# Kernel tuning notes

Measured on AMD Instinct MI355X. Metric: run time of the kernel, lower is better.

The kernel has to match this reference:

```python
import jax, jax.numpy as jnp
import numpy as np

N = 100000   # nodes of ntype 'gene'
E = 800000   # edges per metapath
D = 256      # input_dim == output_dim
H = 4        # attn heads
C = D // H   # out_channels per head
M = 2        # num metapaths (tail relations = M + 1, last = self)


def _lrelu(x):
    return jnp.where(x >= 0, x, 0.2 * x)


def _segment_softmax(logits, seg, num_segments):
    # logits: [E, H], seg: [E] int targets
    mx = jax.ops.segment_max(logits, seg, num_segments=num_segments)
    mx = jnp.where(jnp.isfinite(mx), mx, 0.0)  # empty segments -> 0
    ex = jnp.exp(logits - mx[seg])
    den = jax.ops.segment_sum(ex, seg, num_segments=num_segments)
    return ex / (den[seg] + 1e-16)


def setup_inputs() -> dict:
    key = jax.random.key(0)
    ks = jax.random.split(key, 10)
    s = 1.0 / np.sqrt(D)
    return {
        "x": jax.random.normal(ks[0], (N, D), dtype=jnp.float32),
        "edge_index0": jax.random.randint(ks[1], (2, E), 0, N, dtype=jnp.int32),
        "edge_index1": jax.random.randint(ks[2], (2, E), 0, N, dtype=jnp.int32),
        "W_l": jax.random.normal(ks[3], (D, D), dtype=jnp.float32) * s,
        "b_l": jnp.zeros((D,), dtype=jnp.float32),
        "W_r": jax.random.normal(ks[4], (D, D), dtype=jnp.float32) * s,
        "b_r": jnp.zeros((D,), dtype=jnp.float32),
        "attn": jax.random.normal(ks[5], (M, H, 2 * C), dtype=jnp.float32) * (1.0 / np.sqrt(2 * C)),
        "rel_attn_l": jax.random.normal(ks[6], (H, C), dtype=jnp.float32) * (1.0 / np.sqrt(C)),
        "rel_attn_r": jax.random.normal(ks[7], (H, C), dtype=jnp.float32) * (1.0 / np.sqrt(C)),
    }


def reference(x, edge_index0, edge_index1, W_l, b_l, W_r, b_r, attn, rel_attn_l, rel_attn_r):
    # projections -> [N, H, C]  (eval mode: dropout/batchnorm off)
    l = (x @ W_l.T + b_l).reshape(N, H, C)
    r = (x @ W_r.T + b_r).reshape(N, H, C)

    # attn split: first C for x_i (target, r-proj), last C for x_j (source, l-proj);
    # leaky_relu is elementwise so the concat+dot separates exactly.
    def agg(edge_index, m_idx):
        src, tgt = edge_index[0], edge_index[1]
        a_i = jnp.einsum('ehc,hc->eh', _lrelu(r[tgt]), attn[m_idx, :, :C])
        a_j = jnp.einsum('ehc,hc->eh', _lrelu(l[src]), attn[m_idx, :, C:])
        alpha = _segment_softmax(a_i + a_j, tgt, N)          # [E, H]
        msg = l[src] * alpha[:, :, None]                      # [E, H, C]
        return jax.ops.segment_sum(msg, tgt, num_segments=N)  # [N, H, C]

    out0 = agg(edge_index0, 0)
    out1 = agg(edge_index1, 1)
    emb = jnp.stack([out0, out1, r], axis=1)                  # [N, M+1, H, C]

    # relation-level beta attention (get_beta_weights)
    alpha_l = jnp.einsum('nhc,hc->nh', r, rel_attn_l)         # [N, H]
    alpha_r = jnp.einsum('nrhc,hc->nrh', emb, rel_attn_r)     # [N, M+1, H]
    beta = jax.nn.softmax(_lrelu(alpha_l[:, None, :] + alpha_r), axis=1)

    h = (emb * beta[..., None]).sum(axis=1).reshape(N, D)
    return jax.nn.relu(h)
```

## Files before the change

kernel.cpp:

```cpp
#include <hip/hip_runtime.h>
#include <hip/hip_bf16.h>
#include <math.h>

#define D_ 256
#define H_ 4
#define C_ 64

typedef __attribute__((ext_vector_type(8))) short short8;
typedef __attribute__((ext_vector_type(4))) float f32x4;

__device__ inline float lrelu(float v) { return v >= 0.f ? v : 0.2f * v; }

__device__ inline unsigned short f2b(float f) {
    unsigned u = __float_as_uint(f);
    u = (u + 0x7FFFu + ((u >> 16) & 1u)) >> 16;
    return (unsigned short)u;
}
__device__ inline float b2f(unsigned short u) {
    return __uint_as_float(((unsigned)u) << 16);
}

#define GLDS(src, dst) __builtin_amdgcn_global_load_lds(                      \
    (const __attribute__((address_space(1))) void*)(src),                     \
    (__attribute__((address_space(3))) void*)(dst), 16, 0, 0)

__global__ __launch_bounds__(256) void convert_w(
    const float* __restrict__ Wl, const float* __restrict__ Wr,
    unsigned short* __restrict__ Wb)
{
    int i4 = blockIdx.x * 256 + threadIdx.x;
    float4 v = (i4 < 16384) ? ((const float4*)Wl)[i4]
                            : ((const float4*)Wr)[i4 - 16384];
    ushort4 u;
    u.x = f2b(v.x); u.y = f2b(v.y); u.z = f2b(v.z); u.w = f2b(v.w);
    ((ushort4*)Wb)[i4] = u;
}

__device__ __forceinline__ void stage_a(const float* __restrict__ x, float* dst,
                                        int bm, int k0, int wv, int lane, int Mrows)
{
#pragma unroll
    for (int p = 0; p < 4; p++) {
        int ci = (p * 4 + wv) * 64 + lane;
        int row = ci >> 3, cc = ci & 7;
        int gr = bm + row; if (gr >= Mrows) gr = Mrows - 1;
        const float* src = x + (size_t)gr * 256 + k0 + ((cc ^ (row & 7)) << 2);
        GLDS(src, (char*)dst + (size_t)(p * 4 + wv) * 1024);
    }
}
__device__ __forceinline__ void stage_b(const unsigned short* __restrict__ W,
                                        unsigned short* dst, int bn, int k0,
                                        int wv, int lane)
{
#pragma unroll
    for (int p = 0; p < 2; p++) {
        int ci = (p * 4 + wv) * 64 + lane;
        int col = ci >> 2, cc = ci & 3;
        const unsigned short* src = W + (size_t)(bn + col) * 256 + k0 +
                                    ((cc ^ (col & 3)) << 3);
        GLDS(src, (char*)dst + (size_t)(p * 4 + wv) * 1024);
    }
}

__global__ __launch_bounds__(256) void gemm_fused(
    const float* __restrict__ x, const unsigned short* __restrict__ Wb,
    const float* __restrict__ b_l, const float* __restrict__ b_r,
    unsigned short* __restrict__ lout, float* __restrict__ rout, int Mrows)
{
    __shared__ float As[2][128 * 32];
    __shared__ unsigned short Bs[2][128 * 32];
    const int tid = threadIdx.x;
    const int lane = tid & 63, wv = tid >> 6;
    const int wr = wv >> 1, wc = wv & 1;
    const int sel = blockIdx.x >> 1;
    const int bn = (blockIdx.x & 1) * 128;
    const int bm = blockIdx.y * 128;
    const unsigned short* W = Wb + (size_t)sel * 65536;

    f32x4 acc[4][4];
#pragma unroll
    for (int m = 0; m < 4; m++)
#pragma unroll
        for (int n = 0; n < 4; n++) acc[m][n] = (f32x4)0.f;

    stage_a(x, As[0], bm, 0, wv, lane, Mrows);
    stage_b(W, Bs[0], bn, 0, wv, lane);
    __syncthreads();

    int cur = 0;
#pragma unroll
    for (int t = 0; t < 8; t++) {
        if (t < 7) {
            stage_a(x, As[cur ^ 1], bm, (t + 1) * 32, wv, lane, Mrows);
            stage_b(W, Bs[cur ^ 1], bn, (t + 1) * 32, wv, lane);
        }
        short8 bfr[4];
#pragma unroll
        for (int n = 0; n < 4; n++) {
            int col = wc * 64 + n * 16 + (lane & 15);
            int sc = (lane >> 4) ^ (col & 3);
            bfr[n] = *(const short8*)&Bs[cur][col * 32 + sc * 8];
        }
        short8 afr[4];
#pragma unroll
        for (int m = 0; m < 4; m++) {
            int row = wr * 64 + m * 16 + (lane & 15);
            int c0 = (lane >> 4) * 2;
            const float* ap = &As[cur][row * 32];
            float4 f0 = *(const float4*)&ap[(c0 ^ (row & 7)) << 2];
            float4 f1 = *(const float4*)&ap[((c0 + 1) ^ (row & 7)) << 2];
            union { short8 v; __hip_bfloat162 b2[4]; } u;
            u.b2[0] = __float22bfloat162_rn(make_float2(f0.x, f0.y));
            u.b2[1] = __float22bfloat162_rn(make_float2(f0.z, f0.w));
            u.b2[2] = __float22bfloat162_rn(make_float2(f1.x, f1.y));
            u.b2[3] = __float22bfloat162_rn(make_float2(f1.z, f1.w));
            afr[m] = u.v;
        }
#pragma unroll
        for (int m = 0; m < 4; m++)
#pragma unroll
            for (int n = 0; n < 4; n++)
                acc[m][n] = __builtin_amdgcn_mfma_f32_16x16x32_bf16(
                    afr[m], bfr[n], acc[m][n], 0, 0, 0);
        __syncthreads();
        cur ^= 1;
    }

    const float* bias = sel ? b_r : b_l;
#pragma unroll
    for (int m = 0; m < 4; m++) {
        int grow0 = bm + wr * 64 + m * 16 + (lane >> 4) * 4;
#pragma unroll
        for (int n = 0; n < 4; n++) {
            int gcol = bn + wc * 64 + n * 16 + (lane & 15);
            float bv = bias[gcol];
#pragma unroll
            for (int q = 0; q < 4; q++) {
                int grow = grow0 + q;
                if (grow < Mrows) {
                    float v = acc[m][n][q] + bv;
                    if (sel == 0) lout[(size_t)grow * 256 + gcol] = f2b(v);
                    else          rout[(size_t)grow * 256 + gcol] = v;
                }
            }
        }
    }
}

__global__ __launch_bounds__(256) void node_logits(
    const unsigned short* __restrict__ l, const float* __restrict__ r,
    const float* __restrict__ attn, const float* __restrict__ rel_l,
    const float* __restrict__ rel_r,
    float2* __restrict__ ej2, float* __restrict__ al, float* __restrict__ rd,
    int Nn)
{
    int lane = threadIdx.x & 63;
    int n = blockIdx.x * 4 + (threadIdx.x >> 6);
    if (n >= Nn) return;
    int h = lane >> 4, q = lane & 15;

    ushort4 lv4 = *(const ushort4*)&l[(size_t)n * D_ + lane * 4];
    float4 rv4 = *(const float4*)&r[(size_t)n * D_ + lane * 4];
    float4 a0 = *(const float4*)&attn[(0 * H_ + h) * 128 + 64 + q * 4];
    float4 a1 = *(const float4*)&attn[(1 * H_ + h) * 128 + 64 + q * 4];
    float4 wl = *(const float4*)&rel_l[h * C_ + q * 4];
    float4 wr = *(const float4*)&rel_r[h * C_ + q * 4];

    float lf[4] = { b2f(lv4.x), b2f(lv4.y), b2f(lv4.z), b2f(lv4.w) };
    float rf[4] = { rv4.x, rv4.y, rv4.z, rv4.w };
    float af0[4] = { a0.x, a0.y, a0.z, a0.w };
    float af1[4] = { a1.x, a1.y, a1.z, a1.w };
    float wlf[4] = { wl.x, wl.y, wl.z, wl.w };
    float wrf[4] = { wr.x, wr.y, wr.z, wr.w };

    float v2 = 0.f, v3 = 0.f, v4 = 0.f, v5 = 0.f, v6 = 0.f;
#pragma unroll
    for (int k = 0; k < 4; k++) {
        float ll = lrelu(lf[k]);
        v2 = fmaf(ll, af0[k], v2);
        v3 = fmaf(ll, af1[k], v3);
        v4 = fmaf(rf[k], wlf[k], v4);
        v5 = fmaf(lf[k], wrf[k], v5);
        v6 = fmaf(rf[k], wrf[k], v6);
    }
#pragma unroll
    for (int off = 1; off < 16; off <<= 1) {
        v2 += __shfl_xor(v2, off);
        v3 += __shfl_xor(v3, off);
        v4 += __shfl_xor(v4, off);
        v5 += __shfl_xor(v5, off);
        v6 += __shfl_xor(v6, off);
    }
    if (q == 0) {
        int NH = Nn * H_;
        int nh = n * H_ + h;
        float e0 = __expf(v2), e1 = __expf(v3);
        ej2[nh]      = make_float2(e0, e0 * v5);
        ej2[NH + nh] = make_float2(e1, e1 * v5);
        al[nh] = v4;
        rd[nh] = v6;
    }
}

__global__ __launch_bounds__(256) void edge_hist(
    const int* __restrict__ ei0, const int* __restrict__ ei1,
    int* __restrict__ hist, int E_, int Nn)
{
    int e = blockIdx.x * 256 + threadIdx.x;
    if (e >= E_) return;
    atomicAdd(&hist[ei0[E_ + e]], 1);
    atomicAdd(&hist[Nn + ei1[E_ + e]], 1);
}

__global__ __launch_bounds__(256) void scan_a(
    const int* __restrict__ hist, int* __restrict__ segoff,
    int* __restrict__ bsum, int Nn)
{
    int m = blockIdx.y;
    int gid = blockIdx.x * 256 + threadIdx.x;
    int lane = threadIdx.x & 63, wid = threadIdx.x >> 6;
    int v = (gid < Nn) ? hist[m * Nn + gid] : 0;
    int incl = v;
#pragma unroll
    for (int off = 1; off < 64; off <<= 1) {
        int u = __shfl_up(incl, off);
        if (lane >= off) incl += u;
    }
    __shared__ int ws[4], wo[4];
    if (lane == 63) ws[wid] = incl;
    __syncthreads();
    if (threadIdx.x == 0) {
        int run = 0;
#pragma unroll
        for (int i = 0; i < 4; i++) { wo[i] = run; run += ws[i]; }
        bsum[m * 512 + blockIdx.x] = run;
    }
    __syncthreads();
    if (gid < Nn) segoff[m * Nn + gid] = incl - v + wo[wid];
}

__global__ __launch_bounds__(512) void scan_b(int* __restrict__ bsum, int nb)
{
    int m = blockIdx.x;
    int* b = bsum + m * 512;
    int tid = threadIdx.x, lane = tid & 63, wid = tid >> 6;
    int v = (tid < nb) ? b[tid] : 0;
    int incl = v;
#pragma unroll
    for (int off = 1; off < 64; off <<= 1) {
        int u = __shfl_up(incl, off);
        if (lane >= off) incl += u;
    }
    __shared__ int ws[8], wo[8];
    if (lane == 63) ws[wid] = incl;
    __syncthreads();
    if (tid == 0) {
        int run = 0;
#pragma unroll
        for (int i = 0; i < 8; i++) { wo[i] = run; run += ws[i]; }
    }
    __syncthreads();
    if (tid < nb) b[tid] = incl - v + wo[wid];
}

__global__ __launch_bounds__(256) void scan_c(
    int* __restrict__ segoff, const int* __restrict__ bsum, int Nn)
{
    int m = blockIdx.y;
    int gid = blockIdx.x * 256 + threadIdx.x;
    if (gid < Nn) segoff[m * Nn + gid] += bsum[m * 512 + blockIdx.x];
}

__global__ __launch_bounds__(256) void edge_scatter(
    const int* __restrict__ ei0, const int* __restrict__ ei1,
    const int* __restrict__ segoff, int* __restrict__ cursor,
    int* __restrict__ srcs, int E_, int Nn)
{
    int e = blockIdx.x * 256 + threadIdx.x;
    if (e >= E_) return;
    int t0 = ei0[E_ + e];
    int p0 = segoff[t0] + atomicAdd(&cursor[t0], 1);
    srcs[p0] = ei0[e];
    int t1 = ei1[E_ + e];
    int p1 = segoff[Nn + t1] + atomicAdd(&cursor[Nn + t1], 1);
    srcs[E_ + p1] = ei1[e];
}

__global__ __launch_bounds__(256) void aggregate(
    const int* __restrict__ hist, const int* __restrict__ segoff,
    const int* __restrict__ srcs, const float2* __restrict__ ej2,
    const float* __restrict__ al, const float* __restrict__ rd,
    const float* __restrict__ r, const unsigned short* __restrict__ l,
    float* __restrict__ out, int Nn, int E_)
{
    int lane = threadIdx.x & 63;
    int t = blockIdx.x * 4 + (threadIdx.x >> 6);
    if (t >= Nn) return;
    int h = lane >> 4, q = lane & 15;
    int NH = Nn * H_;
    int nh = t * H_ + h;

    int beg0 = segoff[t],      deg0 = hist[t];
    int beg1 = segoff[Nn + t], deg1 = hist[Nn + t];
    float den0 = 0.f, pn0 = 0.f, den1 = 0.f, pn1 = 0.f;
    for (int j = q; j < deg0; j += 16) {
        float2 v = ej2[(size_t)srcs[beg0 + j] * H_ + h];
        den0 += v.x; pn0 += v.y;
    }
    for (int j = q; j < deg1; j += 16) {
        float2 v = ej2[(size_t)NH + (size_t)srcs[E_ + beg1 + j] * H_ + h];
        den1 += v.x; pn1 += v.y;
    }
#pragma unroll
    for (int off = 1; off < 16; off <<= 1) {
        den0 += __shfl_xor(den0, off); pn0 += __shfl_xor(pn0, off);
        den1 += __shfl_xor(den1, off); pn1 += __shfl_xor(pn1, off);
    }

    float a = al[nh];
    float b0 = lrelu(a + pn0 / (den0 + 1e-16f));
    float b1 = lrelu(a + pn1 / (den1 + 1e-16f));
    float b2 = lrelu(a + rd[nh]);
    float mm = fmaxf(b0, fmaxf(b1, b2));
    float e0 = __expf(b0 - mm), e1 = __expf(b1 - mm), e2 = __expf(b2 - mm);
    float inv = 1.f / (e0 + e1 + e2);
    float wm0 = e0 * inv / (den0 + 1e-16f);
    float wm1 = e1 * inv / (den1 + 1e-16f);
    float b2v = e2 * inv;

    float4 acc = *(const float4*)&r[(size_t)t * D_ + lane * 4];
    acc.x *= b2v; acc.y *= b2v; acc.z *= b2v; acc.w *= b2v;

#pragma unroll
    for (int m = 0; m < 2; m++) {
        const int* sp = srcs + (size_t)m * E_;
        int beg = m ? beg1 : beg0;
        int deg = m ? deg1 : deg0;
        float wmv = m ? wm1 : wm0;
        const float2* ep = ej2 + (size_t)m * NH;
#pragma unroll 4
        for (int j = 0; j < deg; j++) {
            int s = sp[beg + j];
            float w = ep[(size_t)s * H_ + h].x * wmv;
            ushort4 lv = *(const ushort4*)&l[(size_t)s * D_ + lane * 4];
            acc.x = fmaf(b2f(lv.x), w, acc.x);
            acc.y = fmaf(b2f(lv.y), w, acc.y);
            acc.z = fmaf(b2f(lv.z), w, acc.z);
            acc.w = fmaf(b2f(lv.w), w, acc.w);
        }
    }
    float4 o;
    o.x = fmaxf(acc.x, 0.f); o.y = fmaxf(acc.y, 0.f);
    o.z = fmaxf(acc.z, 0.f); o.w = fmaxf(acc.w, 0.f);
    *(float4*)&out[(size_t)t * D_ + lane * 4] = o;
}

extern "C" void kernel_launch(void* const* d_in, const int* in_sizes, int n_in,
                              void* d_out, int out_size, void* d_ws, size_t ws_size,
                              hipStream_t stream) {
    const float* x     = (const float*)d_in[0];
    const int*   ei0   = (const int*)d_in[1];
    const int*   ei1   = (const int*)d_in[2];
    const float* W_l   = (const float*)d_in[3];
    const float* b_l   = (const float*)d_in[4];
    const float* W_r   = (const float*)d_in[5];
    const float* b_r   = (const float*)d_in[6];
    const float* attn  = (const float*)d_in[7];
    const float* rel_l = (const float*)d_in[8];
    const float* rel_r = (const float*)d_in[9];
    float* out = (float*)d_out;

    const int Nn = in_sizes[0] / D_;
    const int E_ = in_sizes[1] / 2;
    const size_t ND = (size_t)Nn * D_;
    const int NH = Nn * H_;

    char* base = (char*)d_ws;
    unsigned short* l = (unsigned short*)base;      size_t off = ND * 2;
    float2* ej2  = (float2*)(base + off); off += (size_t)2 * NH * 8;
    float* al    = (float*)(base + off);  off += (size_t)NH * 4;
    float* rd    = (float*)(base + off);  off += (size_t)NH * 4;
    int* hist    = (int*)(base + off);    off += (size_t)2 * Nn * 4;
    int* cursor  = (int*)(base + off);    off += (size_t)2 * Nn * 4;
    int* segoff  = (int*)(base + off);    off += (size_t)2 * Nn * 4;
    int* bsum    = (int*)(base + off);    off += (size_t)1024 * 4;
    int* srcs    = (int*)(base + off);    off += (size_t)2 * E_ * 4;
    unsigned short* Wb = (unsigned short*)(base + off); off += (size_t)2 * 65536 * 2;

    hipMemsetAsync(hist, 0, (size_t)4 * Nn * 4, stream);

    convert_w<<<128, 256, 0, stream>>>(W_l, W_r, Wb);

    int rowTiles = (Nn + 127) / 128;
    gemm_fused<<<dim3(4, rowTiles), 256, 0, stream>>>(x, Wb, b_l, b_r, l, out, Nn);

    node_logits<<<(Nn + 3) / 4, 256, 0, stream>>>(l, out, attn, rel_l, rel_r,
                                                  ej2, al, rd, Nn);

    int eb = (E_ + 255) / 256;
    int nb = (Nn + 255) / 256;
    edge_hist<<<eb, 256, 0, stream>>>(ei0, ei1, hist, E_, Nn);
    scan_a<<<dim3(nb, 2), 256, 0, stream>>>(hist, segoff, bsum, Nn);
    scan_b<<<2, 512, 0, stream>>>(bsum, nb);
    scan_c<<<dim3(nb, 2), 256, 0, stream>>>(segoff, bsum, Nn);
    edge_scatter<<<eb, 256, 0, stream>>>(ei0, ei1, segoff, cursor, srcs, E_, Nn);

    aggregate<<<(Nn + 3) / 4, 256, 0, stream>>>(
        hist, segoff, srcs, ej2, al, rd, out, l, out, Nn, E_);
}
```

Measured before the change: 482.5 us.

## Fuse softmax denominator pass into aggregation and store r projection as bf16

```diff
diff --git a/kernel.cpp b/kernel.cpp
--- a/kernel.cpp
+++ b/kernel.cpp
@@ -62,10 +62,11 @@
     }
 }
 
+template <bool RB16>
 __global__ __launch_bounds__(256) void gemm_fused(
     const float* __restrict__ x, const unsigned short* __restrict__ Wb,
     const float* __restrict__ b_l, const float* __restrict__ b_r,
-    unsigned short* __restrict__ lout, float* __restrict__ rout, int Mrows)
+    unsigned short* __restrict__ lout, void* __restrict__ rout, int Mrows)
 {
     __shared__ float As[2][128 * 32];
     __shared__ unsigned short Bs[2][128 * 32];
@@ -139,16 +140,21 @@
                 int grow = grow0 + q;
                 if (grow < Mrows) {
                     float v = acc[m][n][q] + bv;
-                    if (sel == 0) lout[(size_t)grow * 256 + gcol] = f2b(v);
-                    else          rout[(size_t)grow * 256 + gcol] = v;
+                    if (sel == 0) {
+                        lout[(size_t)grow * 256 + gcol] = f2b(v);
+                    } else {
+                        if (RB16) ((unsigned short*)rout)[(size_t)grow * 256 + gcol] = f2b(v);
+                        else      ((float*)rout)[(size_t)grow * 256 + gcol] = v;
+                    }
                 }
             }
         }
     }
 }
 
+template <bool RB16>
 __global__ __launch_bounds__(256) void node_logits(
-    const unsigned short* __restrict__ l, const float* __restrict__ r,
+    const unsigned short* __restrict__ l, const void* __restrict__ rv,
     const float* __restrict__ attn, const float* __restrict__ rel_l,
     const float* __restrict__ rel_r,
     float2* __restrict__ ej2, float* __restrict__ al, float* __restrict__ rd,
@@ -160,14 +166,20 @@
     int h = lane >> 4, q = lane & 15;
 
     ushort4 lv4 = *(const ushort4*)&l[(size_t)n * D_ + lane * 4];
-    float4 rv4 = *(const float4*)&r[(size_t)n * D_ + lane * 4];
+    float rf[4];
+    if (RB16) {
+        ushort4 ru = ((const ushort4*)rv)[(size_t)n * 64 + lane];
+        rf[0] = b2f(ru.x); rf[1] = b2f(ru.y); rf[2] = b2f(ru.z); rf[3] = b2f(ru.w);
+    } else {
+        float4 rv4 = ((const float4*)rv)[(size_t)n * 64 + lane];
+        rf[0] = rv4.x; rf[1] = rv4.y; rf[2] = rv4.z; rf[3] = rv4.w;
+    }
     float4 a0 = *(const float4*)&attn[(0 * H_ + h) * 128 + 64 + q * 4];
     float4 a1 = *(const float4*)&attn[(1 * H_ + h) * 128 + 64 + q * 4];
     float4 wl = *(const float4*)&rel_l[h * C_ + q * 4];
     float4 wr = *(const float4*)&rel_r[h * C_ + q * 4];
 
     float lf[4] = { b2f(lv4.x), b2f(lv4.y), b2f(lv4.z), b2f(lv4.w) };
-    float rf[4] = { rv4.x, rv4.y, rv4.z, rv4.w };
     float af0[4] = { a0.x, a0.y, a0.z, a0.w };
     float af1[4] = { a1.x, a1.y, a1.z, a1.w };
     float wlf[4] = { wl.x, wl.y, wl.z, wl.w };
@@ -286,35 +298,50 @@
     srcs[E_ + p1] = ei1[e];
 }
 
+template <bool RB16>
 __global__ __launch_bounds__(256) void aggregate(
     const int* __restrict__ hist, const int* __restrict__ segoff,
     const int* __restrict__ srcs, const float2* __restrict__ ej2,
     const float* __restrict__ al, const float* __restrict__ rd,
-    const float* __restrict__ r, const unsigned short* __restrict__ l,
+    const void* __restrict__ rv, const unsigned short* __restrict__ l,
     float* __restrict__ out, int Nn, int E_)
 {
     int lane = threadIdx.x & 63;
     int t = blockIdx.x * 4 + (threadIdx.x >> 6);
     if (t >= Nn) return;
-    int h = lane >> 4, q = lane & 15;
+    int h = lane >> 4;
     int NH = Nn * H_;
     int nh = t * H_ + h;
 
     int beg0 = segoff[t],      deg0 = hist[t];
     int beg1 = segoff[Nn + t], deg1 = hist[Nn + t];
+
+    float4 acc0 = make_float4(0.f, 0.f, 0.f, 0.f);
+    float4 acc1 = make_float4(0.f, 0.f, 0.f, 0.f);
     float den0 = 0.f, pn0 = 0.f, den1 = 0.f, pn1 = 0.f;
-    for (int j = q; j < deg0; j += 16) {
-        float2 v = ej2[(size_t)srcs[beg0 + j] * H_ + h];
+
+#pragma unroll 4
+    for (int j = 0; j < deg0; j++) {
+        int s = srcs[beg0 + j];
+        float2 v = ej2[(size_t)s * H_ + h];
         den0 += v.x; pn0 += v.y;
-    }
-    for (int j = q; j < deg1; j += 16) {
-        float2 v = ej2[(size_t)NH + (size_t)srcs[E_ + beg1 + j] * H_ + h];
+        ushort4 lv = *(const ushort4*)&l[(size_t)s * D_ + lane * 4];
+        acc0.x = fmaf(b2f(lv.x), v.x, acc0.x);
+        acc0.y = fmaf(b2f(lv.y), v.x, acc0.y);
+        acc0.z = fmaf(b2f(lv.z), v.x, acc0.z);
+        acc0.w = fmaf(b2f(lv.w), v.x, acc0.w);
+    }
+    const float2* ep1 = ej2 + NH;
+#pragma unroll 4
+    for (int j = 0; j < deg1; j++) {
+        int s = srcs[E_ + beg1 + j];
+        float2 v = ep1[(size_t)s * H_ + h];
         den1 += v.x; pn1 += v.y;
-    }
-#pragma unroll
-    for (int off = 1; off < 16; off <<= 1) {
-        den0 += __shfl_xor(den0, off); pn0 += __shfl_xor(pn0, off);
-        den1 += __shfl_xor(den1, off); pn1 += __shfl_xor(pn1, off);
+        ushort4 lv = *(const ushort4*)&l[(size_t)s * D_ + lane * 4];
+        acc1.x = fmaf(b2f(lv.x), v.x, acc1.x);
+        acc1.y = fmaf(b2f(lv.y), v.x, acc1.y);
+        acc1.z = fmaf(b2f(lv.z), v.x, acc1.z);
+        acc1.w = fmaf(b2f(lv.w), v.x, acc1.w);
     }
 
     float a = al[nh];
@@ -328,30 +355,19 @@
     float wm1 = e1 * inv / (den1 + 1e-16f);
     float b2v = e2 * inv;
 
-    float4 acc = *(const float4*)&r[(size_t)t * D_ + lane * 4];
-    acc.x *= b2v; acc.y *= b2v; acc.z *= b2v; acc.w *= b2v;
-
-#pragma unroll
-    for (int m = 0; m < 2; m++) {
-        const int* sp = srcs + (size_t)m * E_;
-        int beg = m ? beg1 : beg0;
-        int deg = m ? deg1 : deg0;
-        float wmv = m ? wm1 : wm0;
-        const float2* ep = ej2 + (size_t)m * NH;
-#pragma unroll 4
-        for (int j = 0; j < deg; j++) {
-            int s = sp[beg + j];
-            float w = ep[(size_t)s * H_ + h].x * wmv;
-            ushort4 lv = *(const ushort4*)&l[(size_t)s * D_ + lane * 4];
-            acc.x = fmaf(b2f(lv.x), w, acc.x);
-            acc.y = fmaf(b2f(lv.y), w, acc.y);
-            acc.z = fmaf(b2f(lv.z), w, acc.z);
-            acc.w = fmaf(b2f(lv.w), w, acc.w);
-        }
-    }
+    float4 rrow;
+    if (RB16) {
+        ushort4 ru = ((const ushort4*)rv)[(size_t)t * 64 + lane];
+        rrow = make_float4(b2f(ru.x), b2f(ru.y), b2f(ru.z), b2f(ru.w));
+    } else {
+        rrow = ((const float4*)rv)[(size_t)t * 64 + lane];
+    }
+
     float4 o;
-    o.x = fmaxf(acc.x, 0.f); o.y = fmaxf(acc.y, 0.f);
-    o.z = fmaxf(acc.z, 0.f); o.w = fmaxf(acc.w, 0.f);
+    o.x = fmaxf(fmaf(wm0, acc0.x, fmaf(wm1, acc1.x, b2v * rrow.x)), 0.f);
+    o.y = fmaxf(fmaf(wm0, acc0.y, fmaf(wm1, acc1.y, b2v * rrow.y)), 0.f);
+    o.z = fmaxf(fmaf(wm0, acc0.z, fmaf(wm1, acc1.z, b2v * rrow.z)), 0.f);
+    o.w = fmaxf(fmaf(wm0, acc0.w, fmaf(wm1, acc1.w, b2v * rrow.w)), 0.f);
     *(float4*)&out[(size_t)t * D_ + lane * 4] = o;
 }
 
@@ -386,16 +402,28 @@
     int* bsum    = (int*)(base + off);    off += (size_t)1024 * 4;
     int* srcs    = (int*)(base + off);    off += (size_t)2 * E_ * 4;
     unsigned short* Wb = (unsigned short*)(base + off); off += (size_t)2 * 65536 * 2;
+    unsigned short* rb = (unsigned short*)(base + off);
+    const bool rb16 = (ws_size >= off + ND * 2);
+    void* r_any = rb16 ? (void*)rb : (void*)out;
 
     hipMemsetAsync(hist, 0, (size_t)4 * Nn * 4, stream);
 
     convert_w<<<128, 256, 0, stream>>>(W_l, W_r, Wb);
 
     int rowTiles = (Nn + 127) / 128;
-    gemm_fused<<<dim3(4, rowTiles), 256, 0, stream>>>(x, Wb, b_l, b_r, l, out, Nn);
-
-    node_logits<<<(Nn + 3) / 4, 256, 0, stream>>>(l, out, attn, rel_l, rel_r,
-                                                  ej2, al, rd, Nn);
+    if (rb16)
+        gemm_fused<true ><<<dim3(4, rowTiles), 256, 0, stream>>>(
+            x, Wb, b_l, b_r, l, r_any, Nn);
+    else
+        gemm_fused<false><<<dim3(4, rowTiles), 256, 0, stream>>>(
+            x, Wb, b_l, b_r, l, r_any, Nn);
+
+    if (rb16)
+        node_logits<true ><<<(Nn + 3) / 4, 256, 0, stream>>>(
+            l, r_any, attn, rel_l, rel_r, ej2, al, rd, Nn);
+    else
+        node_logits<false><<<(Nn + 3) / 4, 256, 0, stream>>>(
+            l, r_any, attn, rel_l, rel_r, ej2, al, rd, Nn);
 
     int eb = (E_ + 255) / 256;
     int nb = (Nn + 255) / 256;
@@ -405,6 +433,10 @@
     scan_c<<<dim3(nb, 2), 256, 0, stream>>>(segoff, bsum, Nn);
     edge_scatter<<<eb, 256, 0, stream>>>(ei0, ei1, segoff, cursor, srcs, E_, Nn);
 
-    aggregate<<<(Nn + 3) / 4, 256, 0, stream>>>(
-        hist, segoff, srcs, ej2, al, rd, out, l, out, Nn, E_);
-}
+    if (rb16)
+        aggregate<true ><<<(Nn + 3) / 4, 256, 0, stream>>>(
+            hist, segoff, srcs, ej2, al, rd, r_any, l, out, Nn, E_);
+    else
+        aggregate<false><<<(Nn + 3) / 4, 256, 0, stream>>>(
+            hist, segoff, srcs, ej2, al, rd, r_any, l, out, Nn, E_);
+}
```

After: 459.7 us. -4.7%, faster.
